# Kernel tuning notes

Measured on AMD Instinct MI355X. Metric: run time of the kernel, lower is better.

Reference implementation:

```python
import jax, jax.numpy as jnp
import numpy as np

G_RATIO = 0.5
TMAX = 0.25
TB_FACTOR = 0.001


def conv2d(x, w, b):
    # x: [B,C,H,W], w: [O,C,kh,kw]
    y = jax.lax.conv_general_dilated(x, w, (1, 1), 'SAME',
                                     dimension_numbers=('NCHW', 'OIHW', 'NCHW'))
    return y + b[None, :, None, None]


def encoder(inputs, w1, b1, w2, b2):
    # simplified cost-map encoder standing in for smp.Unet; outputs sigmoid cost map [B,1,H,W]
    h = jax.nn.relu(conv2d(inputs, w1, b1))
    return jax.nn.sigmoid(conv2d(h, w2, b2))


def get_heuristic(goal_maps, tb_factor=TB_FACTOR):
    # goal_maps: [B,H,W] one-hot
    B, H, W = goal_maps.shape
    yy, xx = jnp.meshgrid(jnp.arange(H), jnp.arange(W), indexing='ij')
    loc = jnp.stack([yy, xx], 0).astype(goal_maps.dtype)          # [2,H,W]
    goal_loc = jnp.einsum('kij,bij->bk', loc, goal_maps)           # [B,2]
    d = jnp.abs(loc[None] - goal_loc[:, :, None, None])            # [B,2,H,W]
    h = d.min(axis=1) + d.max(axis=1)                              # chebyshev-style
    euc = jnp.sqrt((d ** 2).sum(axis=1))
    return h + tb_factor * euc


def st_softmax_noexp(val):
    # straight-through hard selection of the max-probability node
    B = val.shape[0]
    v = val.reshape(B, -1)
    y = v / v.sum(-1, keepdims=True)
    ind = jnp.argmax(y, axis=-1)
    y_hard = jax.nn.one_hot(ind, y.shape[-1], dtype=y.dtype)
    return (jax.lax.stop_gradient(y_hard - y) + y).reshape(val.shape)


def backtrack(start_maps, goal_maps, parents, current_t):
    B, H, W = start_maps.shape
    par = jax.lax.stop_gradient(parents).astype(jnp.int32)         # [B,HW]
    goal_flat = goal_maps.reshape(B, -1).astype(jnp.int32)
    path = goal_flat
    loc = (par * goal_flat).sum(-1)                                # parent of goal node
    rng = jnp.arange(B)

    def body(i, carry):
        path, loc = carry
        path = path.at[rng, loc].set(1)
        loc = par[rng, loc]
        return (path, loc)

    path, _ = jax.lax.fori_loop(0, current_t, body, (path, loc))
    return path.reshape(B, H, W).astype(jnp.float32)


def differentiable_astar(cost_maps, start_maps, goal_maps, obstacles_maps):
    cost = cost_maps[:, 0]
    start = start_maps[:, 0]
    goal = goal_maps[:, 0]
    obs = obstacles_maps[:, 0]
    B, H, W = cost.shape

    # Moore (8-neighbor) expansion filter: 3x3 ones with zero center
    nf = jnp.ones((1, 1, 3, 3), cost.dtype).at[0, 0, 1, 1].set(0.0)

    def expand(x):  # x: [B,H,W]
        return jax.lax.conv_general_dilated(x[:, None], nf, (1, 1), 'SAME',
                                            dimension_numbers=('NCHW', 'OIHW', 'NCHW'))[:, 0]

    h = get_heuristic(goal) + cost
    size = W
    steps = int(TMAX * H * W)
    inv_sqrt = 1.0 / np.sqrt(size)

    goal_idx = jnp.argmax(goal.reshape(B, -1), -1).astype(cost.dtype)
    parents0 = jnp.broadcast_to(goal_idx[:, None], (B, H * W)).astype(cost.dtype)
    one = jnp.asarray(1.0, cost.dtype)

    def step(carry, _):
        g, open_m, hist, parents = carry
        f = G_RATIO * g + (1.0 - G_RATIO) * h
        f_exp = jnp.exp(-f * inv_sqrt) * open_m
        sel = st_softmax_noexp(f_exp)                              # [B,H,W]

        dist_to_goal = (sel * goal).sum((1, 2), keepdims=True)
        is_unsolved = (dist_to_goal < 1e-8).astype(cost.dtype)

        hist = jnp.clip(hist + sel, 0.0, 1.0)
        open_m = jnp.clip(open_m - is_unsolved * sel, 0.0, 1.0)

        nbr = expand(sel) * obs
        g2 = expand((g + cost) * sel)
        idx = ((one - open_m) * (one - hist) + open_m * (g > g2).astype(cost.dtype)) * nbr
        idx = jax.lax.stop_gradient(idx)
        g = g2 * idx + g * (one - idx)
        g = jax.lax.stop_gradient(g)                               # detach_g=True
        open_m = jax.lax.stop_gradient(jnp.clip(open_m + idx, 0.0, 1.0))

        idx_f = idx.reshape(B, -1)
        new_par = jnp.argmax(sel.reshape(B, -1), -1).astype(cost.dtype)[:, None]
        parents = new_par * idx_f + parents * (one - idx_f)
        return (g, open_m, hist, parents), None

    init = (jnp.zeros_like(cost), start, jnp.zeros_like(cost), parents0)
    (g, open_m, hist, parents), _ = jax.lax.scan(step, init, None, length=steps)

    paths = backtrack(start, goal, parents, steps - 1)
    return hist[:, None], paths[:, None]


def setup_inputs() -> dict:
    key = jax.random.key(0)
    k1, k2, k3, k4, k5 = jax.random.split(key, 5)
    B, H, W = 64, 32, 32
    maps = (jax.random.uniform(k1, (B, 1, H, W)) > 0.15).astype(jnp.float32)  # 1 = free
    sidx = jax.random.randint(k2, (B,), 0, H * W)
    gidx = jax.random.randint(k3, (B,), 0, H * W)
    start = jax.nn.one_hot(sidx, H * W, dtype=jnp.float32).reshape(B, 1, H, W)
    goal = jax.nn.one_hot(gidx, H * W, dtype=jnp.float32).reshape(B, 1, H, W)
    maps = jnp.clip(maps + start + goal, 0.0, 1.0)  # ensure start/goal are free
    w1 = jax.random.normal(k4, (32, 2, 3, 3), jnp.float32) * 0.1
    b1 = jnp.zeros((32,), jnp.float32)
    w2 = jax.random.normal(k5, (1, 32, 3, 3), jnp.float32) * 0.1
    b2 = jnp.zeros((1,), jnp.float32)
    return {"map_designs": maps, "start_maps": start, "goal_maps": goal,
            "w1": w1, "b1": b1, "w2": w2, "b2": b2}


def reference(map_designs, start_maps, goal_maps, w1, b1, w2, b2):
    # encoder_input='m+': concat map with start+goal
    inputs = jnp.concatenate([map_designs, start_maps + goal_maps], axis=1)
    pred_cost_maps = encoder(inputs, w1, b1, w2, b2)
    obstacles_maps = map_designs  # ignore_obstacles=True, learn_obstacles=False
    histories, paths = differentiable_astar(pred_cost_maps, start_maps, goal_maps, obstacles_maps)
    return histories, paths, pred_cost_maps
```

## Files before the change

kernel.cpp:

```cpp
#include <hip/hip_runtime.h>


#define HW 1024

#define DPP_MAX64(key, ctrl) do {                                              \
    unsigned int _lo = (unsigned int)(key);                                    \
    unsigned int _hi = (unsigned int)((key) >> 32);                            \
    unsigned int _slo = (unsigned int)__builtin_amdgcn_update_dpp(             \
        (int)_lo, (int)_lo, (ctrl), 0xf, 0xf, false);                          \
    unsigned int _shi = (unsigned int)__builtin_amdgcn_update_dpp(             \
        (int)_hi, (int)_hi, (ctrl), 0xf, 0xf, false);                          \
    unsigned long long _o = ((unsigned long long)_shi << 32) | _slo;           \
    if (_o > (key)) (key) = _o;                                                \
} while (0)

__global__ __launch_bounds__(256) void fused_nastar(
    const float* __restrict__ maps, const float* __restrict__ start,
    const float* __restrict__ goal, const float* __restrict__ w1,
    const float* __restrict__ b1, const float* __restrict__ w2,
    const float* __restrict__ b2, float* __restrict__ out_hist,
    float* __restrict__ out_path, float* __restrict__ out_cost) {
  __shared__ float hid[8][HW];
  __shared__ float c_l[HW];
  __shared__ float g_l[HW];
  __shared__ float h_l[HW];
  __shared__ unsigned int vkey[HW];
  __shared__ unsigned short par[HW];
  __shared__ unsigned char path_sh[HW];
  __shared__ unsigned int hist_lds[64];

  const int t = threadIdx.x;
  const int b = blockIdx.x;
  const float C_INV = 0.17677669529663687f;

  const float* m_p = maps  + b * HW;
  const float* s_p = start + b * HW;
  const float* g_p = goal  + b * HW;

  float acc2[4] = {b2[0], b2[0], b2[0], b2[0]};
  for (int grp = 0; grp < 4; ++grp) {
    #pragma unroll
    for (int p = 0; p < 4; ++p) {
      int pix = p * 256 + t;
      int y = pix >> 5, x = pix & 31;
      float win0[9], win1[9];
      #pragma unroll
      for (int ky = 0; ky < 3; ++ky) {
        #pragma unroll
        for (int kx = 0; kx < 3; ++kx) {
          int yy = y + ky - 1, xx = x + kx - 1;
          bool ok = (yy >= 0) && (yy <= 31) && (xx >= 0) && (xx <= 31);
          int q = ok ? yy * 32 + xx : 0;
          float v0 = m_p[q];
          float v1 = s_p[q] + g_p[q];
          win0[ky * 3 + kx] = ok ? v0 : 0.0f;
          win1[ky * 3 + kx] = ok ? v1 : 0.0f;
        }
      }
      #pragma unroll
      for (int ocl = 0; ocl < 8; ++ocl) {
        int oc = grp * 8 + ocl;
        const float* w = w1 + oc * 18;
        float acc = b1[oc];
        #pragma unroll
        for (int k = 0; k < 9; ++k) {
          acc += win0[k] * w[k];
          acc += win1[k] * w[9 + k];
        }
        hid[ocl][pix] = fmaxf(acc, 0.0f);
      }
    }
    __syncthreads();
    #pragma unroll
    for (int p = 0; p < 4; ++p) {
      int pix = p * 256 + t;
      int y = pix >> 5, x = pix & 31;
      float a = acc2[p];
      #pragma unroll
      for (int ocl = 0; ocl < 8; ++ocl) {
        int ic = grp * 8 + ocl;
        const float* w = w2 + ic * 9;
        #pragma unroll
        for (int ky = 0; ky < 3; ++ky) {
          #pragma unroll
          for (int kx = 0; kx < 3; ++kx) {
            int yy = y + ky - 1, xx = x + kx - 1;
            bool ok = (yy >= 0) && (yy <= 31) && (xx >= 0) && (xx <= 31);
            int q = ok ? yy * 32 + xx : 0;
            float hv = hid[ocl][q];
            a += (ok ? hv : 0.0f) * w[ky * 3 + kx];
          }
        }
      }
      acc2[p] = a;
    }
    __syncthreads();
  }
  #pragma unroll
  for (int p = 0; p < 4; ++p) {
    int pix = p * 256 + t;
    float c = 1.0f / (1.0f + expf(-acc2[p]));
    c_l[pix] = c;
    out_cost[b * HW + pix] = c;
  }
  __syncthreads();

  if (t < 64) {
    const int lane = t;
    reinterpret_cast<int4*>(path_sh)[lane] = make_int4(0, 0, 0, 0);
    int myg = -1;
    #pragma unroll
    for (int j = 0; j < 16; ++j) {
      int cell = j * 64 + lane;
      if (g_p[cell] > 0.5f) myg = cell;
    }
    unsigned long long gm = __ballot(myg >= 0);
    int src_lane = (int)__ffsll(gm) - 1;
    const int goal_idx = __shfl(myg, src_lane, 64);
    const int gy = goal_idx >> 5, gx = goal_idx & 31;

    unsigned int open_m = 0, hist_m = 0, obs_m = 0;
    #pragma unroll
    for (int j = 0; j < 16; ++j) {
      int cell = j * 64 + lane;
      int y = cell >> 5, x = cell & 31;
      float cst = c_l[cell];
      int dy = y - gy; dy = dy < 0 ? -dy : dy;
      int dx = x - gx; dx = dx < 0 ? -dx : dx;
      float e = sqrtf((float)(dy * dy + dx * dx));
      float heur = __fadd_rn((float)(dy + dx), __fmul_rn(0.001f, e));
      float hc = __fadd_rn(heur, cst);
      h_l[cell] = hc;
      g_l[cell] = 0.0f;
      bool isobs = (m_p[cell] != 0.0f);
      bool isst  = (s_p[cell] > 0.5f);
      if (isobs) obs_m  |= 1u << j;
      if (isst)  open_m |= 1u << j;
      float f = 0.5f * (0.0f + hc);
      float ex = expf(__fmul_rn(-f, C_INV));
      vkey[cell] = isst ? __float_as_uint(ex) : 0u;
      par[cell] = (unsigned short)goal_idx;
    }

    const int x = lane & 31, half = lane >> 5;
    const unsigned int lowbase = 1023u - (unsigned)lane;

    for (int step = 0; step < 256; ++step) {
      unsigned long long k[16];
      #pragma unroll
      for (int j = 0; j < 16; ++j) {
        unsigned int v = vkey[j * 64 + lane];
        k[j] = ((unsigned long long)v << 32) | (lowbase - 64u * (unsigned)j);
      }
      #pragma unroll
      for (int s = 8; s >= 1; s >>= 1) {
        #pragma unroll
        for (int i = 0; i < s; ++i)
          if (k[i + s] > k[i]) k[i] = k[i + s];
      }
      unsigned long long key = k[0];
      DPP_MAX64(key, 0x111);
      DPP_MAX64(key, 0x112);
      DPP_MAX64(key, 0x114);
      DPP_MAX64(key, 0x118);
      DPP_MAX64(key, 0x142);
      DPP_MAX64(key, 0x143);
      unsigned int klo =
          (unsigned int)__builtin_amdgcn_readlane((int)(unsigned int)key, 63);
      const int sel = __builtin_amdgcn_readfirstlane(1023 - (int)klo);
      const int jsel = sel >> 6, owner = sel & 63;
      const int ys = sel >> 5, xs = sel & 31;
      const bool unsolved = (sel != goal_idx);

      int dxs = x - xs; int adx = dxs < 0 ? -dxs : dxs;
      const bool act = (adx <= 1);
      const bool samep = (((ys ^ half) & 1) == 0);
      const int yA = samep ? ys : (ys - 1);
      const bool vAv = act && (samep ? (adx >= 1) : (yA >= 0));
      const int yB = ys + 1;
      const bool vBv = act && (!samep) && (yB <= 31);
      const int cA = vAv ? (yA * 32 + x) : 0;
      const int cB = vBv ? (yB * 32 + x) : 0;

      float gs = g_l[sel];
      float cs = c_l[sel];
      float gA = g_l[cA], hA = h_l[cA];
      float gB = g_l[cB], hB = h_l[cB];

      const float gsum = gs + cs;
      const int vjA = yA >> 1;
      const int jB  = yB >> 1;

      bool obA = (obs_m  >> (vjA & 15)) & 1;
      bool opA = (open_m >> (vjA & 15)) & 1;
      bool hiA = (hist_m >> (vjA & 15)) & 1;
      bool obB = (obs_m  >> (jB  & 15)) & 1;
      bool opB = (open_m >> (jB  & 15)) & 1;
      bool hiB = (hist_m >> (jB  & 15)) & 1;

      const bool idxA = vAv && obA && ((!opA && !hiA) || (opA && (gA > gsum)));
      const bool idxB = vBv && obB && ((!opB && !hiB) || (opB && (gB > gsum)));
      const bool ownerlane = (lane == owner);
      const bool closeU = unsolved && ownerlane;

      const bool histnew = ownerlane && !((hist_m >> (jsel & 15)) & 1);
      const bool opencl  = closeU && ((open_m >> (jsel & 15)) & 1);

      hist_m |= ownerlane ? (1u << (jsel & 15)) : 0u;
      unsigned int clr = closeU ? (1u << (jsel & 15)) : 0u;
      unsigned int aA  = idxA ? (1u << (vjA & 15)) : 0u;
      unsigned int aB  = idxB ? (1u << (jB  & 15)) : 0u;
      open_m = (open_m & ~clr) | aA | aB;

      if (closeU) vkey[sel] = 0u;
      float fA = 0.5f * (gsum + hA);
      unsigned int nvA = __float_as_uint(expf(__fmul_rn(-fA, C_INV)));
      float fB = 0.5f * (gsum + hB);
      unsigned int nvB = __float_as_uint(expf(__fmul_rn(-fB, C_INV)));
      if (idxA) { g_l[cA] = gsum; vkey[cA] = nvA; par[cA] = (unsigned short)sel; }
      if (idxB) { g_l[cB] = gsum; vkey[cB] = nvB; par[cB] = (unsigned short)sel; }

      unsigned long long anych = __ballot(idxA || idxB || histnew || opencl);
      if (anych == 0ull) break;
    }

    hist_lds[lane] = hist_m;

    if (lane == 0) {
      path_sh[goal_idx] = 1;
      int loc = par[goal_idx];
      for (int i = 0; i < 255; ++i) {
        if (path_sh[loc]) break;
        path_sh[loc] = 1;
        loc = par[loc];
      }
    }
  }
  __syncthreads();

  const int base = t * 4;
  float hv[4], pv[4];
  #pragma unroll
  for (int p = 0; p < 4; ++p) {
    int cell = base + p;
    hv[p] = (float)((hist_lds[cell & 63] >> (cell >> 6)) & 1);
    pv[p] = (float)path_sh[cell];
  }
  *reinterpret_cast<float4*>(out_hist + b * HW + base) =
      make_float4(hv[0], hv[1], hv[2], hv[3]);
  *reinterpret_cast<float4*>(out_path + b * HW + base) =
      make_float4(pv[0], pv[1], pv[2], pv[3]);
}

extern "C" void kernel_launch(void* const* d_in, const int* in_sizes, int n_in,
                              void* d_out, int out_size, void* d_ws, size_t ws_size,
                              hipStream_t stream) {
  (void)in_sizes; (void)n_in; (void)d_ws; (void)ws_size; (void)out_size;
  const float* maps  = (const float*)d_in[0];
  const float* start = (const float*)d_in[1];
  const float* goal  = (const float*)d_in[2];
  const float* w1    = (const float*)d_in[3];
  const float* b1    = (const float*)d_in[4];
  const float* w2    = (const float*)d_in[5];
  const float* b2    = (const float*)d_in[6];

  float* out      = (float*)d_out;
  float* out_hist = out;
  float* out_path = out + 64 * HW;
  float* out_cost = out + 128 * HW;

  fused_nastar<<<64, 256, 0, stream>>>(maps, start, goal, w1, b1, w2, b2,
                                       out_hist, out_path, out_cost);
}
```

Baseline: 133.7 us.

## Keep A* search state in per-lane registers instead of shared memory

Moves the g, h, cost and priority-key arrays of the single-wavefront A* loop from LDS into per-lane register arrays of 16 entries. Neighbour values are picked with unrolled predicated selects over the two candidate row-pairs, and the selected node's g and cost are broadcast with readlane. The per-lane max reduction now compares 32-bit values with a tracked index instead of 64-bit keys. This removes LDS load/store latency from the serial critical loop, at the cost of more VGPRs and extra select instructions.

Measured after the change: 156.1 us. 1.17x slower.

```diff
diff --git a/kernel.cpp b/kernel.cpp
--- a/kernel.cpp
+++ b/kernel.cpp
@@ -22,9 +22,6 @@
     float* __restrict__ out_path, float* __restrict__ out_cost) {
   __shared__ float hid[8][HW];
   __shared__ float c_l[HW];
-  __shared__ float g_l[HW];
-  __shared__ float h_l[HW];
-  __shared__ unsigned int vkey[HW];
   __shared__ unsigned short par[HW];
   __shared__ unsigned char path_sh[HW];
   __shared__ unsigned int hist_lds[64];
@@ -120,25 +117,28 @@
     const int gy = goal_idx >> 5, gx = goal_idx & 31;
 
     unsigned int open_m = 0, hist_m = 0, obs_m = 0;
+    float gr[16], hr[16], cr[16];
+    unsigned int vr[16];
     #pragma unroll
     for (int j = 0; j < 16; ++j) {
       int cell = j * 64 + lane;
       int y = cell >> 5, x = cell & 31;
       float cst = c_l[cell];
+      cr[j] = cst;
       int dy = y - gy; dy = dy < 0 ? -dy : dy;
       int dx = x - gx; dx = dx < 0 ? -dx : dx;
       float e = sqrtf((float)(dy * dy + dx * dx));
       float heur = __fadd_rn((float)(dy + dx), __fmul_rn(0.001f, e));
       float hc = __fadd_rn(heur, cst);
-      h_l[cell] = hc;
-      g_l[cell] = 0.0f;
+      hr[j] = hc;
+      gr[j] = 0.0f;
       bool isobs = (m_p[cell] != 0.0f);
       bool isst  = (s_p[cell] > 0.5f);
       if (isobs) obs_m  |= 1u << j;
       if (isst)  open_m |= 1u << j;
       float f = 0.5f * (0.0f + hc);
       float ex = expf(__fmul_rn(-f, C_INV));
-      vkey[cell] = isst ? __float_as_uint(ex) : 0u;
+      vr[j] = isst ? __float_as_uint(ex) : 0u;
       par[cell] = (unsigned short)goal_idx;
     }
 
@@ -146,19 +146,21 @@
     const unsigned int lowbase = 1023u - (unsigned)lane;
 
     for (int step = 0; step < 256; ++step) {
-      unsigned long long k[16];
-      #pragma unroll
-      for (int j = 0; j < 16; ++j) {
-        unsigned int v = vkey[j * 64 + lane];
-        k[j] = ((unsigned long long)v << 32) | (lowbase - 64u * (unsigned)j);
-      }
-      #pragma unroll
-      for (int s = 8; s >= 1; s >>= 1) {
+      unsigned int tv[8], tj[8];
+      #pragma unroll
+      for (int i = 0; i < 8; ++i) {
+        bool gt2 = vr[i + 8] > vr[i];
+        tv[i] = gt2 ? vr[i + 8] : vr[i];
+        tj[i] = gt2 ? (unsigned)(i + 8) : (unsigned)i;
+      }
+      #pragma unroll
+      for (int s = 4; s >= 1; s >>= 1) {
         #pragma unroll
         for (int i = 0; i < s; ++i)
-          if (k[i + s] > k[i]) k[i] = k[i + s];
-      }
-      unsigned long long key = k[0];
+          if (tv[i + s] > tv[i]) { tv[i] = tv[i + s]; tj[i] = tj[i + s]; }
+      }
+      unsigned long long key = ((unsigned long long)tv[0] << 32) |
+                               (unsigned long long)(lowbase - (tj[0] << 6));
       DPP_MAX64(key, 0x111);
       DPP_MAX64(key, 0x112);
       DPP_MAX64(key, 0x114);
@@ -172,6 +174,30 @@
       const int ys = sel >> 5, xs = sel & 31;
       const bool unsolved = (sel != goal_idx);
 
+      const int j0  = (ys > 0 ? ys - 1 : 0) >> 1;
+      const int j1u = (j0 < 15) ? j0 + 1 : 15;
+      const int jP  = (ys < 31 ? ys + 1 : 31) >> 1;
+      const bool jS_is_j0 = (jsel == j0);
+      const bool jP_is_j0 = (jP == j0);
+
+      float gj0 = 0.f, hj0 = 0.f, cj0 = 0.f, gj1 = 0.f, hj1 = 0.f, cj1 = 0.f;
+      #pragma unroll
+      for (int j = 0; j < 16; ++j) {
+        if (j0 == j) {
+          const int jn = (j < 15) ? j + 1 : 15;
+          gj0 = gr[j];  hj0 = hr[j];  cj0 = cr[j];
+          gj1 = gr[jn]; hj1 = hr[jn]; cj1 = cr[jn];
+        }
+      }
+
+      float gselv = jS_is_j0 ? gj0 : gj1;
+      float cselv = jS_is_j0 ? cj0 : cj1;
+      float gs = __uint_as_float((unsigned int)__builtin_amdgcn_readlane(
+          (int)__float_as_uint(gselv), owner));
+      float cs = __uint_as_float((unsigned int)__builtin_amdgcn_readlane(
+          (int)__float_as_uint(cselv), owner));
+      const float gsum = gs + cs;
+
       int dxs = x - xs; int adx = dxs < 0 ? -dxs : dxs;
       const bool act = (adx <= 1);
       const bool samep = (((ys ^ half) & 1) == 0);
@@ -182,21 +208,19 @@
       const int cA = vAv ? (yA * 32 + x) : 0;
       const int cB = vBv ? (yB * 32 + x) : 0;
 
-      float gs = g_l[sel];
-      float cs = c_l[sel];
-      float gA = g_l[cA], hA = h_l[cA];
-      float gB = g_l[cB], hB = h_l[cB];
-
-      const float gsum = gs + cs;
-      const int vjA = yA >> 1;
-      const int jB  = yB >> 1;
+      const bool vjA_is_j0 = (!samep) || jS_is_j0;
+      const int vjA = samep ? jsel : j0;
+      float gA = vjA_is_j0 ? gj0 : gj1;
+      float hA = vjA_is_j0 ? hj0 : hj1;
+      float gB = jP_is_j0 ? gj0 : gj1;
+      float hB = jP_is_j0 ? hj0 : hj1;
 
       bool obA = (obs_m  >> (vjA & 15)) & 1;
       bool opA = (open_m >> (vjA & 15)) & 1;
       bool hiA = (hist_m >> (vjA & 15)) & 1;
-      bool obB = (obs_m  >> (jB  & 15)) & 1;
-      bool opB = (open_m >> (jB  & 15)) & 1;
-      bool hiB = (hist_m >> (jB  & 15)) & 1;
+      bool obB = (obs_m  >> (jP & 15)) & 1;
+      bool opB = (open_m >> (jP & 15)) & 1;
+      bool hiB = (hist_m >> (jP & 15)) & 1;
 
       const bool idxA = vAv && obA && ((!opA && !hiA) || (opA && (gA > gsum)));
       const bool idxB = vBv && obB && ((!opB && !hiB) || (opB && (gB > gsum)));
@@ -209,16 +233,33 @@
       hist_m |= ownerlane ? (1u << (jsel & 15)) : 0u;
       unsigned int clr = closeU ? (1u << (jsel & 15)) : 0u;
       unsigned int aA  = idxA ? (1u << (vjA & 15)) : 0u;
-      unsigned int aB  = idxB ? (1u << (jB  & 15)) : 0u;
+      unsigned int aB  = idxB ? (1u << (jP & 15)) : 0u;
       open_m = (open_m & ~clr) | aA | aB;
 
-      if (closeU) vkey[sel] = 0u;
       float fA = 0.5f * (gsum + hA);
       unsigned int nvA = __float_as_uint(expf(__fmul_rn(-fA, C_INV)));
       float fB = 0.5f * (gsum + hB);
       unsigned int nvB = __float_as_uint(expf(__fmul_rn(-fB, C_INV)));
-      if (idxA) { g_l[cA] = gsum; vkey[cA] = nvA; par[cA] = (unsigned short)sel; }
-      if (idxB) { g_l[cB] = gsum; vkey[cB] = nvB; par[cB] = (unsigned short)sel; }
+
+      if (idxA) par[cA] = (unsigned short)sel;
+      if (idxB) par[cB] = (unsigned short)sel;
+
+      #pragma unroll
+      for (int j = 0; j < 16; ++j) {
+        const bool hit = (j == j0) || (j == j1u);
+        if (hit) {
+          const bool atlo = (j == j0);
+          const bool uA = idxA && (vjA_is_j0 == atlo);
+          const bool uB = idxB && (jP_is_j0 == atlo);
+          const bool uu = uA || uB;
+          if (uu) gr[j] = gsum;
+          unsigned int nv = uA ? nvA : nvB;
+          if (uu) vr[j] = nv;
+          if (j == jsel) {
+            if (closeU) vr[j] = 0u;
+          }
+        }
+      }
 
       unsigned long long anych = __ballot(idxA || idxB || histnew || opencl);
       if (anych == 0ull) break;
```
